# Kernel optimization log

Hardware: AMD Instinct MI355X
Metric: run time of the kernel (lower is better)

The kernel has to match this reference:

```python
import jax, jax.numpy as jnp
import numpy as np

Q = 8
T, N, M = 16, 128, 128
K = 5
C_IN = 2 + T            # x, y, and T solution timesteps stacked as channels
C_HID = 2 * (4 + Q)     # 24
C_OUT = 4 + Q           # kappa, v1, v2, f, q RK-stage fields
DT = 1.0


def _conv(h, W, b):
    # h: (C, N, M), W: (O, C, K, K) -> (O, N, M), SAME padding (padding = K//2)
    o = jax.lax.conv_general_dilated(h[None], W, (1, 1), 'SAME',
                                     dimension_numbers=('NCHW', 'OIHW', 'NCHW'))[0]
    return o + b[:, None, None]


def setup_inputs() -> dict:
    key = jax.random.key(0)
    ks = jax.random.split(key, 12)
    def w(k, o, c):
        return jax.random.normal(k, (o, c, K, K), jnp.float32) * (1.0 / np.sqrt(c * K * K))
    return {
        'x': jax.random.normal(ks[0], (N, M), jnp.float32),
        'y': jax.random.normal(ks[1], (N, M), jnp.float32),
        'u': jax.random.normal(ks[2], (T, N, M), jnp.float32),
        'W1': w(ks[3], C_HID, C_IN), 'b1': jnp.zeros((C_HID,), jnp.float32),
        'W2': w(ks[4], C_HID, C_HID), 'b2': jnp.zeros((C_HID,), jnp.float32),
        'W3': w(ks[5], C_HID, C_HID), 'b3': jnp.zeros((C_HID,), jnp.float32),
        'W4': w(ks[6], C_HID, C_HID), 'b4': jnp.zeros((C_HID,), jnp.float32),
        'W5': w(ks[7], C_OUT, C_HID), 'b5': jnp.zeros((C_OUT,), jnp.float32),
        'rk_A': jax.random.normal(ks[8], (Q, Q), jnp.float32) * 0.05,
        'rk_b': jax.random.normal(ks[9], (Q,), jnp.float32) * 0.05,
    }


def reference(x, y, u, W1, b1, W2, b2, W3, b3, W4, b4, W5, b5, rk_A, rk_b):
    def net(xx, yy):
        h = jnp.concatenate([xx[None], yy[None], u], axis=0)  # (2+T, N, M)
        h = jax.nn.relu(_conv(h, W1, b1))
        h = jax.nn.relu(_conv(h, W2, b2))
        h = jax.nn.relu(_conv(h, W3, b3))
        h = jax.nn.relu(_conv(h, W4, b4))
        return _conv(h, W5, b5)  # (C_OUT, N, M)

    outs, vjp = jax.vjp(net, x, y)
    kappa, v1, v2, f = outs[0], outs[1], outs[2], outs[3]
    u_rk = outs[4:]  # (Q, N, M)

    # one-hot channel cotangents for kappa, v1, v2 and the Q RK-stage fields
    idx = jnp.array([0, 1, 2] + list(range(4, 4 + Q)))
    n_cot = idx.shape[0]
    cots = jnp.zeros((n_cot, C_OUT, N, M), outs.dtype).at[jnp.arange(n_cot), idx].set(1.0)

    # batched first-order VJPs (replaces the torch autograd.grad loop)
    gx, gy = jax.vmap(vjp)(cots)
    kappa_x, v1_x, v2_x = gx[0], gx[1], gx[2]
    kappa_y, v1_y, v2_y = gy[0], gy[1], gy[2]
    u_rk_x, u_rk_y = gx[3:], gy[3:]  # (Q, N, M)

    ones = jnp.ones((N, M), outs.dtype)
    cot_u = cots[3:]

    def du_x(xx, c):
        return jax.vjp(lambda a: net(a, y), xx)[1](c)[0]

    def du_y(yy, c):
        return jax.vjp(lambda a: net(x, a), yy)[1](c)[0]

    # second derivatives: VJP of the first-derivative map, batched over RK stages
    u_rk_xx = jax.vmap(lambda c: jax.vjp(lambda a: du_x(a, c), x)[1](ones)[0])(cot_u)
    u_rk_yy = jax.vmap(lambda c: jax.vjp(lambda a: du_y(a, c), y)[1](ones)[0])(cot_u)

    pde = (kappa[None] * (u_rk_xx + u_rk_yy)
           + kappa_x[None] * u_rk_x + kappa_y[None] * u_rk_y
           + v1[None] * u_rk_x + v2[None] * u_rk_y
           + f[None])

    uhat_i = u_rk + DT * jnp.einsum('ij,jkl->ikl', rk_A, pde)
    uhat_f = u_rk + DT * jnp.einsum('ij,jkl->ikl', rk_A - rk_b[None, :], pde)

    # all outputs of the torch forward, stacked along channel dim: (2Q+10, N, M)
    return jnp.concatenate([
        uhat_i, uhat_f,
        kappa[None], kappa_x[None], kappa_y[None],
        v1[None], v1_x[None], v1_y[None],
        v2[None], v2_x[None], v2_y[None],
        f[None]], axis=0)
```

## Files before the change

### kernel.cpp

```cpp
#include <hip/hip_runtime.h>

static constexpr int P = 16384;

static constexpr int OFF_H1   = 0;
static constexpr int OFF_H2   = 24 * P;
static constexpr int OFF_H3   = 48 * P;
static constexpr int OFF_H4   = 72 * P;
static constexpr int OFF_OUT5 = 96 * P;
static constexpr int OFF_GA   = 108 * P;
static constexpr int OFF_GB   = 372 * P;
static constexpr int OFF_DXY  = 636 * P;
static constexpr int OFF_W    = 658 * P;

static constexpr int PW1 = 0;
static constexpr int PW2 = 10800;
static constexpr int PW3 = 25200;
static constexpr int PW4 = 39600;
static constexpr int PW5 = 54000;
static constexpr int PB4 = 61200;
static constexpr int PB3 = 75600;
static constexpr int PB2 = 90000;
static constexpr int PB1 = 104400;

__global__ void pack_weights(const float* __restrict__ W1, const float* __restrict__ W2,
                             const float* __restrict__ W3, const float* __restrict__ W4,
                             const float* __restrict__ W5, float* __restrict__ wp,
                             float* __restrict__ tbl) {
    int i = blockIdx.x * 256 + threadIdx.x;
    if (i < 10800) {
        int co = i % 24, ci = (i / 24) % 18, t = i / 432;
        wp[PW1 + i] = W1[(co * 18 + ci) * 25 + t];
    }
    if (i < 14400) {
        int co = i % 24, ci = (i / 24) % 24, t = i / 576;
        wp[PW2 + i] = W2[(co * 24 + ci) * 25 + t];
        wp[PW3 + i] = W3[(co * 24 + ci) * 25 + t];
        wp[PW4 + i] = W4[(co * 24 + ci) * 25 + t];
        int cin = i % 24, cout = (i / 24) % 24, tb = i / 576;
        wp[PB4 + i] = W4[(cout * 24 + cin) * 25 + (24 - tb)];
        wp[PB3 + i] = W3[(cout * 24 + cin) * 25 + (24 - tb)];
        wp[PB2 + i] = W2[(cout * 24 + cin) * 25 + (24 - tb)];
    }
    if (i < 7200) {
        int co = i % 12, ci = (i / 12) % 24, t = i / 288;
        wp[PW5 + i] = W5[(co * 24 + ci) * 25 + t];
    }
    if (i < 1200) {
        int ci = i % 2, co = (i / 2) % 24, t = i / 48;
        wp[PB1 + i] = W1[(co * 18 + ci) * 25 + (24 - t)];
    }
    if (i < 6600) {
        int cx = i % 5, cy = (i / 5) % 5, ci = (i / 25) % 24, cot = i / 600;
        int oc = (cot < 3) ? cot : cot + 1;
        int a0 = (cy <= 2) ? 0 : cy - 2, a1 = (cy >= 2) ? 4 : cy + 2;
        int b0 = (cx <= 2) ? 0 : cx - 2, b1 = (cx >= 2) ? 4 : cx + 2;
        const float* __restrict__ w = W5 + (oc * 24 + ci) * 25;
        float s = 0.f;
        for (int a = a0; a <= a1; ++a)
            for (int b = b0; b <= b1; ++b) s += w[a * 5 + b];
        tbl[i] = s;
    }
}

__global__ void stage_input(const float* __restrict__ x, const float* __restrict__ y,
                            const float* __restrict__ u, float* __restrict__ in18) {
    int i = blockIdx.x * 256 + threadIdx.x;
    int pl = i / P, p = i - pl * P;
    float v = (pl == 0) ? x[p] : (pl == 1) ? y[p] : u[(pl - 2) * P + p];
    in18[i] = v;
}

template <int TH, int CIN, int CHUNK, int COUT_TOT, int COB,
          bool RELU, bool MASK, bool BATCH, bool TBL>
__global__ __launch_bounds__(TH * 16, 7) void conv5x5(
    const float* __restrict__ inbase, const float* __restrict__ wp,
    const float* __restrict__ bias, const float* __restrict__ maskbase,
    const float* __restrict__ tbl, float* __restrict__ outbase) {
    constexpr int NSPL = COUT_TOT / COB;
    constexpr int HR = TH + 4;
    constexpr int NT = TH * 16;
    const int z = blockIdx.z;
    const int half = z % NSPL;
    const int cot = z / NSPL;
    const float* in = inbase + ((BATCH && !TBL) ? cot * CIN * P : 0);
    float* out = outbase + (BATCH ? cot * COUT_TOT * P : 0);
    const int cobase = half * COB;

    __shared__ float smem[CHUNK][HR][20];
    const int tid = threadIdx.x;
    const int bx = blockIdx.x, by = blockIdx.y;
    const int ty = tid >> 4, tx = tid & 15;

    float acc[COB];
#pragma unroll
    for (int co = 0; co < COB; ++co) acc[co] = bias ? bias[cobase + co] : 0.f;

    for (int c0 = 0; c0 < CIN; c0 += CHUNK) {
        if (c0) __syncthreads();
        for (int i = tid; i < CHUNK * HR * 20; i += NT) {
            int ci = i / (HR * 20), rem = i - ci * (HR * 20);
            int r = rem / 20, c = rem - r * 20;
            int gy = by * TH + r - 2, gx = bx * 16 + c - 2;
            float v = 0.f;
            if ((unsigned)gy < 128u && (unsigned)gx < 128u) {
                if (TBL) {
                    float m = in[(c0 + ci) * P + gy * 128 + gx];
                    if (m > 0.f) {
                        int cy = (gy < 2) ? gy : (gy > 125) ? gy - 123 : 2;
                        int cx = (gx < 2) ? gx : (gx > 125) ? gx - 123 : 2;
                        v = tbl[((cot * CIN + c0 + ci) * 5 + cy) * 5 + cx];
                    }
                } else {
                    v = in[(c0 + ci) * P + gy * 128 + gx];
                }
            }
            smem[ci][r][c] = v;
        }
        __syncthreads();

        for (int a = 0; a < 5; ++a) {
            for (int b = 0; b < 5; ++b) {
                const float* __restrict__ wrow =
                    wp + ((a * 5 + b) * CIN + c0) * COUT_TOT + cobase;
                for (int ci = 0; ci < CHUNK; ++ci) {
                    float v = smem[ci][ty + a][tx + b];
#pragma unroll
                    for (int co = 0; co < COB; ++co)
                        acc[co] = fmaf(v, wrow[ci * COUT_TOT + co], acc[co]);
                }
            }
        }
    }

    const int gy = by * TH + ty, gx = bx * 16 + tx, gp = gy * 128 + gx;
#pragma unroll
    for (int co = 0; co < COB; ++co) {
        float v = acc[co];
        if (RELU) v = v > 0.f ? v : 0.f;
        if (MASK) v = (maskbase[(cobase + co) * P + gp] > 0.f) ? v : 0.f;
        out[(cobase + co) * P + gp] = v;
    }
}

__global__ __launch_bounds__(256) void finalize(const float* __restrict__ ws,
                                                const float* __restrict__ rkA,
                                                const float* __restrict__ rkb,
                                                float* __restrict__ outp) {
    const int p = blockIdx.x * 256 + threadIdx.x;
    const float* o5 = ws + OFF_OUT5;
    const float* dxy = ws + OFF_DXY;

    const float kap = o5[0 * P + p], v1 = o5[1 * P + p];
    const float v2  = o5[2 * P + p], f  = o5[3 * P + p];
    const float kx  = dxy[0 * P + p], ky  = dxy[1 * P + p];
    const float v1x = dxy[2 * P + p], v1y = dxy[3 * P + p];
    const float v2x = dxy[4 * P + p], v2y = dxy[5 * P + p];
    const float cx = kx + v1, cy = ky + v2;

    float pde[8], urk[8];
#pragma unroll
    for (int q = 0; q < 8; ++q) {
        urk[q] = o5[(4 + q) * P + p];
        float ux = dxy[(6 + 2 * q) * P + p];
        float uy = dxy[(7 + 2 * q) * P + p];
        pde[q] = fmaf(cx, ux, fmaf(cy, uy, f));
    }
#pragma unroll
    for (int r = 0; r < 8; ++r) {
        float si = 0.f, sf = 0.f;
#pragma unroll
        for (int j = 0; j < 8; ++j) {
            float a = rkA[r * 8 + j];
            si = fmaf(a, pde[j], si);
            sf = fmaf(a - rkb[j], pde[j], sf);
        }
        outp[r * P + p] = urk[r] + si;
        outp[(8 + r) * P + p] = urk[r] + sf;
    }
    outp[16 * P + p] = kap;
    outp[17 * P + p] = kx;
    outp[18 * P + p] = ky;
    outp[19 * P + p] = v1;
    outp[20 * P + p] = v1x;
    outp[21 * P + p] = v1y;
    outp[22 * P + p] = v2;
    outp[23 * P + p] = v2x;
    outp[24 * P + p] = v2y;
    outp[25 * P + p] = f;
}

extern "C" void kernel_launch(void* const* d_in, const int* in_sizes, int n_in,
                              void* d_out, int out_size, void* d_ws, size_t ws_size,
                              hipStream_t stream) {
    const float* x   = (const float*)d_in[0];
    const float* y   = (const float*)d_in[1];
    const float* u   = (const float*)d_in[2];
    const float* W1  = (const float*)d_in[3];
    const float* b1  = (const float*)d_in[4];
    const float* W2  = (const float*)d_in[5];
    const float* b2  = (const float*)d_in[6];
    const float* W3  = (const float*)d_in[7];
    const float* b3  = (const float*)d_in[8];
    const float* W4  = (const float*)d_in[9];
    const float* b4  = (const float*)d_in[10];
    const float* W5  = (const float*)d_in[11];
    const float* b5  = (const float*)d_in[12];
    const float* rkA = (const float*)d_in[13];
    const float* rkb = (const float*)d_in[14];

    float* ws   = (float*)d_ws;
    float* outp = (float*)d_out;
    float* wp   = ws + OFF_W;
    float* tbl  = ws + OFF_GA;

    pack_weights<<<dim3(57), dim3(256), 0, stream>>>(W1, W2, W3, W4, W5, wp, tbl);
    stage_input<<<dim3(18 * 64), dim3(256), 0, stream>>>(x, y, u, ws + OFF_GB);

    dim3 blk256(256), blk128(128);
    conv5x5<16, 18, 9, 24, 4, true, false, false, false><<<dim3(8, 8, 6), blk256, 0, stream>>>(
        ws + OFF_GB, wp + PW1, b1, nullptr, nullptr, ws + OFF_H1);
    conv5x5<16, 24, 12, 24, 4, true, false, false, false><<<dim3(8, 8, 6), blk256, 0, stream>>>(
        ws + OFF_H1, wp + PW2, b2, nullptr, nullptr, ws + OFF_H2);
    conv5x5<16, 24, 12, 24, 4, true, false, false, false><<<dim3(8, 8, 6), blk256, 0, stream>>>(
        ws + OFF_H2, wp + PW3, b3, nullptr, nullptr, ws + OFF_H3);
    conv5x5<16, 24, 12, 24, 4, true, false, false, false><<<dim3(8, 8, 6), blk256, 0, stream>>>(
        ws + OFF_H3, wp + PW4, b4, nullptr, nullptr, ws + OFF_H4);
    conv5x5<16, 24, 12, 12, 4, false, false, false, false><<<dim3(8, 8, 3), blk256, 0, stream>>>(
        ws + OFF_H4, wp + PW5, b5, nullptr, nullptr, ws + OFF_OUT5);

    conv5x5<8, 24, 12, 24, 12, false, true, true, true><<<dim3(8, 16, 22), blk128, 0, stream>>>(
        ws + OFF_H4, wp + PB4, nullptr, ws + OFF_H3, tbl, ws + OFF_GB);
    conv5x5<8, 24, 12, 24, 12, false, true, true, false><<<dim3(8, 16, 22), blk128, 0, stream>>>(
        ws + OFF_GB, wp + PB3, nullptr, ws + OFF_H2, nullptr, ws + OFF_GA);
    conv5x5<8, 24, 12, 24, 12, false, true, true, false><<<dim3(8, 16, 22), blk128, 0, stream>>>(
        ws + OFF_GA, wp + PB2, nullptr, ws + OFF_H1, nullptr, ws + OFF_GB);
    conv5x5<8, 24, 12, 2, 2, false, false, true, false><<<dim3(8, 16, 11), blk128, 0, stream>>>(
        ws + OFF_GB, wp + PB1, nullptr, nullptr, nullptr, ws + OFF_DXY);

    finalize<<<dim3(64), blk256, 0, stream>>>(ws, rkA, rkb, outp);
}
```

Before: 584.8 us.

## Add multi-row register blocking and configurable tile shape to conv5x5

Generalizes the conv kernel so the tile width, the rows per thread and the shared-memory row stride are template parameters. Each thread can now accumulate R output rows, so every weight load is reused across several pixels. The forward layers switch to 8-wide tiles with 8 output channels per block. The batched backward layers compute 2 rows per thread with 12 channels. This cuts weight loads per FMA and changes the grid sizes, at the cost of more registers and different occupancy, and narrower tiles add halo overhead.

```diff
diff --git a/kernel.cpp b/kernel.cpp
--- a/kernel.cpp
+++ b/kernel.cpp
@@ -70,15 +70,17 @@
     in18[i] = v;
 }
 
-template <int TH, int CIN, int CHUNK, int COUT_TOT, int COB,
+template <int NTY, int TW, int R, int SW, int CIN, int CHUNK, int COUT_TOT, int COB,
           bool RELU, bool MASK, bool BATCH, bool TBL>
-__global__ __launch_bounds__(TH * 16, 7) void conv5x5(
+__global__ __launch_bounds__(NTY * TW, 7) void conv5x5(
     const float* __restrict__ inbase, const float* __restrict__ wp,
     const float* __restrict__ bias, const float* __restrict__ maskbase,
     const float* __restrict__ tbl, float* __restrict__ outbase) {
     constexpr int NSPL = COUT_TOT / COB;
-    constexpr int HR = TH + 4;
-    constexpr int NT = TH * 16;
+    constexpr int TR = NTY * R;
+    constexpr int HR = TR + 4;
+    constexpr int HC = TW + 4;
+    constexpr int NT = NTY * TW;
     const int z = blockIdx.z;
     const int half = z % NSPL;
     const int cot = z / NSPL;
@@ -86,21 +88,23 @@
     float* out = outbase + (BATCH ? cot * COUT_TOT * P : 0);
     const int cobase = half * COB;
 
-    __shared__ float smem[CHUNK][HR][20];
+    __shared__ float smem[CHUNK][HR][SW];
     const int tid = threadIdx.x;
     const int bx = blockIdx.x, by = blockIdx.y;
-    const int ty = tid >> 4, tx = tid & 15;
-
-    float acc[COB];
-#pragma unroll
-    for (int co = 0; co < COB; ++co) acc[co] = bias ? bias[cobase + co] : 0.f;
+    const int ty = tid / TW, tx = tid % TW;
+
+    float acc[R][COB];
+#pragma unroll
+    for (int k = 0; k < R; ++k)
+#pragma unroll
+        for (int co = 0; co < COB; ++co) acc[k][co] = bias ? bias[cobase + co] : 0.f;
 
     for (int c0 = 0; c0 < CIN; c0 += CHUNK) {
         if (c0) __syncthreads();
-        for (int i = tid; i < CHUNK * HR * 20; i += NT) {
-            int ci = i / (HR * 20), rem = i - ci * (HR * 20);
-            int r = rem / 20, c = rem - r * 20;
-            int gy = by * TH + r - 2, gx = bx * 16 + c - 2;
+        for (int i = tid; i < CHUNK * HR * HC; i += NT) {
+            int ci = i / (HR * HC), rem = i - ci * (HR * HC);
+            int r = rem / HC, c = rem - r * HC;
+            int gy = by * TR + r - 2, gx = bx * TW + c - 2;
             float v = 0.f;
             if ((unsigned)gy < 128u && (unsigned)gx < 128u) {
                 if (TBL) {
@@ -123,22 +127,32 @@
                 const float* __restrict__ wrow =
                     wp + ((a * 5 + b) * CIN + c0) * COUT_TOT + cobase;
                 for (int ci = 0; ci < CHUNK; ++ci) {
-                    float v = smem[ci][ty + a][tx + b];
-#pragma unroll
-                    for (int co = 0; co < COB; ++co)
-                        acc[co] = fmaf(v, wrow[ci * COUT_TOT + co], acc[co]);
+                    float v[R];
+#pragma unroll
+                    for (int k = 0; k < R; ++k)
+                        v[k] = smem[ci][ty + k * NTY + a][tx + b];
+#pragma unroll
+                    for (int co = 0; co < COB; ++co) {
+                        float w = wrow[ci * COUT_TOT + co];
+#pragma unroll
+                        for (int k = 0; k < R; ++k)
+                            acc[k][co] = fmaf(v[k], w, acc[k][co]);
+                    }
                 }
             }
         }
     }
 
-    const int gy = by * TH + ty, gx = bx * 16 + tx, gp = gy * 128 + gx;
-#pragma unroll
-    for (int co = 0; co < COB; ++co) {
-        float v = acc[co];
-        if (RELU) v = v > 0.f ? v : 0.f;
-        if (MASK) v = (maskbase[(cobase + co) * P + gp] > 0.f) ? v : 0.f;
-        out[(cobase + co) * P + gp] = v;
+#pragma unroll
+    for (int k = 0; k < R; ++k) {
+        const int gy = by * TR + ty + k * NTY, gx = bx * TW + tx, gp = gy * 128 + gx;
+#pragma unroll
+        for (int co = 0; co < COB; ++co) {
+            float v = acc[k][co];
+            if (RELU) v = v > 0.f ? v : 0.f;
+            if (MASK) v = (maskbase[(cobase + co) * P + gp] > 0.f) ? v : 0.f;
+            out[(cobase + co) * P + gp] = v;
+        }
     }
 }
 
@@ -216,25 +230,34 @@
     pack_weights<<<dim3(57), dim3(256), 0, stream>>>(W1, W2, W3, W4, W5, wp, tbl);
     stage_input<<<dim3(18 * 64), dim3(256), 0, stream>>>(x, y, u, ws + OFF_GB);
 
-    dim3 blk256(256), blk128(128);
-    conv5x5<16, 18, 9, 24, 4, true, false, false, false><<<dim3(8, 8, 6), blk256, 0, stream>>>(
+    dim3 blk128(128), blk256(256);
+    conv5x5<16, 8, 1, 12, 18, 9, 24, 8, true, false, false, false>
+        <<<dim3(16, 8, 3), blk128, 0, stream>>>(
         ws + OFF_GB, wp + PW1, b1, nullptr, nullptr, ws + OFF_H1);
-    conv5x5<16, 24, 12, 24, 4, true, false, false, false><<<dim3(8, 8, 6), blk256, 0, stream>>>(
+    conv5x5<16, 8, 1, 12, 24, 12, 24, 8, true, false, false, false>
+        <<<dim3(16, 8, 3), blk128, 0, stream>>>(
         ws + OFF_H1, wp + PW2, b2, nullptr, nullptr, ws + OFF_H2);
-    conv5x5<16, 24, 12, 24, 4, true, false, false, false><<<dim3(8, 8, 6), blk256, 0, stream>>>(
+    conv5x5<16, 8, 1, 12, 24, 12, 24, 8, true, false, false, false>
+        <<<dim3(16, 8, 3), blk128, 0, stream>>>(
         ws + OFF_H2, wp + PW3, b3, nullptr, nullptr, ws + OFF_H3);
-    conv5x5<16, 24, 12, 24, 4, true, false, false, false><<<dim3(8, 8, 6), blk256, 0, stream>>>(
+    conv5x5<16, 8, 1, 12, 24, 12, 24, 8, true, false, false, false>
+        <<<dim3(16, 8, 3), blk128, 0, stream>>>(
         ws + OFF_H3, wp + PW4, b4, nullptr, nullptr, ws + OFF_H4);
-    conv5x5<16, 24, 12, 12, 4, false, false, false, false><<<dim3(8, 8, 3), blk256, 0, stream>>>(
+    conv5x5<16, 8, 1, 12, 24, 12, 12, 6, false, false, false, false>
+        <<<dim3(16, 8, 2), blk128, 0, stream>>>(
         ws + OFF_H4, wp + PW5, b5, nullptr, nullptr, ws + OFF_OUT5);
 
-    conv5x5<8, 24, 12, 24, 12, false, true, true, true><<<dim3(8, 16, 22), blk128, 0, stream>>>(
+    conv5x5<8, 16, 2, 24, 24, 12, 24, 12, false, true, true, true>
+        <<<dim3(8, 8, 22), blk128, 0, stream>>>(
         ws + OFF_H4, wp + PB4, nullptr, ws + OFF_H3, tbl, ws + OFF_GB);
-    conv5x5<8, 24, 12, 24, 12, false, true, true, false><<<dim3(8, 16, 22), blk128, 0, stream>>>(
+    conv5x5<8, 16, 2, 24, 24, 12, 24, 12, false, true, true, false>
+        <<<dim3(8, 8, 22), blk128, 0, stream>>>(
         ws + OFF_GB, wp + PB3, nullptr, ws + OFF_H2, nullptr, ws + OFF_GA);
-    conv5x5<8, 24, 12, 24, 12, false, true, true, false><<<dim3(8, 16, 22), blk128, 0, stream>>>(
+    conv5x5<8, 16, 2, 24, 24, 12, 24, 12, false, true, true, false>
+        <<<dim3(8, 8, 22), blk128, 0, stream>>>(
         ws + OFF_GA, wp + PB2, nullptr, ws + OFF_H1, nullptr, ws + OFF_GB);
-    conv5x5<8, 24, 12, 2, 2, false, false, true, false><<<dim3(8, 16, 11), blk128, 0, stream>>>(
+    conv5x5<8, 16, 1, 24, 24, 12, 2, 2, false, false, true, false>
+        <<<dim3(8, 16, 11), blk128, 0, stream>>>(
         ws + OFF_GB, wp + PB1, nullptr, nullptr, nullptr, ws + OFF_DXY);
 
     finalize<<<dim3(64), blk256, 0, stream>>>(ws, rkA, rkb, outp);
```

Measured after the change: 832.1 us. 1.42x slower.
